# Performance work log

Measured on AMD Instinct MI355X. Metric: run time of the kernel, lower is better.

## Reference

```python
import jax, jax.numpy as jnp
import numpy as np

N_NODES = 50000
N_EDGES = 800000
IN_DIM = 128
HIDDEN = 128
N_CLASSES = 10
BN_EPS = 1e-5


def _sage_conv(x, src, dst, n, w_l, b_l, w_r):
    # PyG SAGEConv (mean aggr): out = lin_l(mean_{j->i} x_j) + lin_r(x_i)
    msg = x[src]  # [E, d] gather
    s = jax.ops.segment_sum(msg, dst, num_segments=n)
    cnt = jax.ops.segment_sum(jnp.ones((src.shape[0], 1), x.dtype), dst, num_segments=n)
    mean = s / jnp.maximum(cnt, 1.0)
    return mean @ w_l.T + b_l + x @ w_r.T


def _bn_eval(x, gamma, beta, mean, var):
    return (x - mean) * (gamma * jax.lax.rsqrt(var + BN_EPS)) + beta


def setup_inputs() -> dict:
    key = jax.random.key(0)
    ks = jax.random.split(key, 16)
    h2 = HIDDEN // 2

    def lin(k, fan_out, fan_in):
        bound = 1.0 / np.sqrt(fan_in)
        return jax.random.uniform(k, (fan_out, fan_in), jnp.float32, -bound, bound)

    return {
        "x": jax.random.normal(ks[0], (N_NODES, IN_DIM), jnp.float32),
        "edge_index": jax.random.randint(ks[1], (2, N_EDGES), 0, N_NODES, jnp.int64),
        "w1l": lin(ks[2], HIDDEN, IN_DIM),
        "b1l": jnp.zeros((HIDDEN,), jnp.float32),
        "w1r": lin(ks[3], HIDDEN, IN_DIM),
        "bn1_gamma": jax.random.uniform(ks[4], (HIDDEN,), jnp.float32, 0.5, 1.5),
        "bn1_beta": jax.random.normal(ks[5], (HIDDEN,), jnp.float32) * 0.1,
        "bn1_mean": jax.random.normal(ks[6], (HIDDEN,), jnp.float32) * 0.1,
        "bn1_var": jax.random.uniform(ks[7], (HIDDEN,), jnp.float32, 0.5, 1.5),
        "w2l": lin(ks[8], h2, HIDDEN),
        "b2l": jnp.zeros((h2,), jnp.float32),
        "w2r": lin(ks[9], h2, HIDDEN),
        "bn2_gamma": jax.random.uniform(ks[10], (h2,), jnp.float32, 0.5, 1.5),
        "bn2_beta": jax.random.normal(ks[11], (h2,), jnp.float32) * 0.1,
        "bn2_mean": jax.random.normal(ks[12], (h2,), jnp.float32) * 0.1,
        "bn2_var": jax.random.uniform(ks[13], (h2,), jnp.float32, 0.5, 1.5),
        "head_w": lin(ks[14], N_CLASSES, h2),
        "head_b": jnp.zeros((N_CLASSES,), jnp.float32),
    }


def reference(x, edge_index, w1l, b1l, w1r, bn1_gamma, bn1_beta, bn1_mean, bn1_var,
              w2l, b2l, w2r, bn2_gamma, bn2_beta, bn2_mean, bn2_var, head_w, head_b):
    src, dst = edge_index[0], edge_index[1]
    n = x.shape[0]
    h = _sage_conv(x, src, dst, n, w1l, b1l, w1r)
    h = jax.nn.relu(_bn_eval(h, bn1_gamma, bn1_beta, bn1_mean, bn1_var))
    # dropout p=0.1 is identity in eval mode
    h = _sage_conv(h, src, dst, n, w2l, b2l, w2r)
    h = jax.nn.relu(_bn_eval(h, bn2_gamma, bn2_beta, bn2_mean, bn2_var))
    return h @ head_w.T + head_b
```

## Files before the change

### kernel.cpp

```cpp
#include <hip/hip_runtime.h>

typedef _Float16 f16;
typedef _Float16 f16x2 __attribute__((ext_vector_type(2)));
typedef _Float16 f16x8 __attribute__((ext_vector_type(8)));
typedef float f32x4 __attribute__((ext_vector_type(4)));

#define N_NODES 50000
#define N_EDGES 800000
#define N_CLASSES 10
#define CAP 64
#define EDGE_BLOCKS ((N_EDGES + 255) / 256)
#define XCVT_BLOCKS (N_NODES * 128 / 8 / 256)

__global__ void zero_cnt_kernel(int* __restrict__ cnt) {
    int i = blockIdx.x * 256 + threadIdx.x;
    if (i < N_NODES / 4) ((int4*)cnt)[i] = make_int4(0, 0, 0, 0);
}

__global__ void build_fused_kernel(const int* __restrict__ src, const int* __restrict__ dst,
                                   int* __restrict__ cnt, unsigned short* __restrict__ bucket,
                                   const float* __restrict__ x,
                                   const float* __restrict__ w1l, const float* __restrict__ w1r,
                                   const float* __restrict__ w2l, const float* __restrict__ w2r,
                                   f16* __restrict__ xh, f16* __restrict__ W1, f16* __restrict__ W2cat) {
    int bid = blockIdx.x;
    if (bid < 2 * EDGE_BLOCKS) {
        int half = bid >> 1;
        if ((bid & 1) == 0) {
            int e = half * 256 + threadIdx.x;
            if (e < N_EDGES) {
                int d = dst[e];
                int s = atomicAdd(&cnt[d], 1);
                if (s < CAP) bucket[(long long)d * CAP + s] = (unsigned short)src[e];
            }
        } else {
            long long base = ((long long)half * 256 + threadIdx.x) * 8;
            float4 a = *(const float4*)(x + base);
            float4 b = *(const float4*)(x + base + 4);
            f16x8 o;
            o[0] = (f16)a.x; o[1] = (f16)a.y; o[2] = (f16)a.z; o[3] = (f16)a.w;
            o[4] = (f16)b.x; o[5] = (f16)b.y; o[6] = (f16)b.z; o[7] = (f16)b.w;
            *(f16x8*)(xh + base) = o;
        }
    } else {
        int wt = (bid - 2 * EDGE_BLOCKS) * 256 + threadIdx.x;
        for (int idx = wt; idx < 128 * 256; idx += 1024) {
            int n = idx >> 8, k = idx & 255;
            W1[idx] = (f16)(k < 128 ? w1l[n * 128 + k] : w1r[n * 128 + k - 128]);
        }
        for (int idx = wt; idx < 128 * 128; idx += 1024) {
            int n = idx >> 7, k = idx & 127;
            W2cat[idx] = (f16)(n < 64 ? w2l[n * 128 + k] : w2r[(n - 64) * 128 + k]);
        }
    }
}

__global__ void agg_mean_f16_kernel(const f16* __restrict__ feat,
                                    const int* __restrict__ cnt,
                                    const unsigned short* __restrict__ bucket,
                                    f16* __restrict__ outb) {
    int node = blockIdx.x * 4 + (threadIdx.x >> 6);
    int lane = threadIdx.x & 63;
    if (node >= N_NODES) return;
    int deg = cnt[node];
    int n_it = deg < CAP ? deg : CAP;
    const unsigned short* b = bucket + (long long)node * CAP;
    int myidx = (lane < n_it) ? (int)b[lane] : 0;
    const f16x2* f2 = (const f16x2*)feat;
    float ax = 0.f, ay = 0.f;
    int j = 0;
    for (; j + 8 <= n_it; j += 8) {
        f16x2 v0 = f2[(long long)__shfl(myidx, j + 0) * 64 + lane];
        f16x2 v1 = f2[(long long)__shfl(myidx, j + 1) * 64 + lane];
        f16x2 v2 = f2[(long long)__shfl(myidx, j + 2) * 64 + lane];
        f16x2 v3 = f2[(long long)__shfl(myidx, j + 3) * 64 + lane];
        f16x2 v4 = f2[(long long)__shfl(myidx, j + 4) * 64 + lane];
        f16x2 v5 = f2[(long long)__shfl(myidx, j + 5) * 64 + lane];
        f16x2 v6 = f2[(long long)__shfl(myidx, j + 6) * 64 + lane];
        f16x2 v7 = f2[(long long)__shfl(myidx, j + 7) * 64 + lane];
        ax += (((float)v0[0] + (float)v1[0]) + ((float)v2[0] + (float)v3[0]))
            + (((float)v4[0] + (float)v5[0]) + ((float)v6[0] + (float)v7[0]));
        ay += (((float)v0[1] + (float)v1[1]) + ((float)v2[1] + (float)v3[1]))
            + (((float)v4[1] + (float)v5[1]) + ((float)v6[1] + (float)v7[1]));
    }
    for (; j + 4 <= n_it; j += 4) {
        f16x2 v0 = f2[(long long)__shfl(myidx, j + 0) * 64 + lane];
        f16x2 v1 = f2[(long long)__shfl(myidx, j + 1) * 64 + lane];
        f16x2 v2 = f2[(long long)__shfl(myidx, j + 2) * 64 + lane];
        f16x2 v3 = f2[(long long)__shfl(myidx, j + 3) * 64 + lane];
        ax += ((float)v0[0] + (float)v1[0]) + ((float)v2[0] + (float)v3[0]);
        ay += ((float)v0[1] + (float)v1[1]) + ((float)v2[1] + (float)v3[1]);
    }
    for (; j < n_it; j++) {
        f16x2 v = f2[(long long)__shfl(myidx, j) * 64 + lane];
        ax += (float)v[0];
        ay += (float)v[1];
    }
    float inv = 1.f / fmaxf((float)deg, 1.f);
    f16x2 r;
    r[0] = (f16)(ax * inv);
    r[1] = (f16)(ay * inv);
    ((f16x2*)outb)[(long long)node * 64 + lane] = r;
}

__global__ __launch_bounds__(256) void sage1_y2_kernel(
    const f16* __restrict__ Am,
    const f16* __restrict__ Ax,
    const f16* __restrict__ W1,
    const float* __restrict__ bias,
    const float* __restrict__ gamma,
    const float* __restrict__ beta,
    const float* __restrict__ bmean,
    const float* __restrict__ bvar,
    const f16* __restrict__ W2cat,
    f16* __restrict__ y2)
{
    __shared__ f16 ldsA[4][32][136];

    int tid  = threadIdx.x;
    int wave = tid >> 6;
    int lane = tid & 63;
    int m_base = blockIdx.x * 128 + wave * 32;
    int lrow = lane & 15;
    int lchunk = lane >> 4;

    f32x4 acc[2][8] = {};

#pragma unroll
    for (int phase = 0; phase < 2; phase++) {
        const f16* A = phase ? Ax : Am;
        const f16* Wp = W1 + phase * 128;

        f16x8 afrag[4][2];
#pragma unroll
        for (int kc = 0; kc < 4; kc++)
#pragma unroll
            for (int mf = 0; mf < 2; mf++) {
                int row = m_base + mf * 16 + lrow;
                row = row < N_NODES ? row : N_NODES - 1;
                afrag[kc][mf] = *(const f16x8*)(A + (long long)row * 128 + kc * 32 + lchunk * 8);
            }

#pragma unroll
        for (int nf = 0; nf < 8; nf++) {
#pragma unroll
            for (int kc = 0; kc < 4; kc++) {
                f16x8 b = *(const f16x8*)(Wp + (long long)(nf * 16 + lrow) * 256
                                          + kc * 32 + lchunk * 8);
                acc[0][nf] = __builtin_amdgcn_mfma_f32_16x16x32_f16(afrag[kc][0], b, acc[0][nf], 0, 0, 0);
                acc[1][nf] = __builtin_amdgcn_mfma_f32_16x16x32_f16(afrag[kc][1], b, acc[1][nf], 0, 0, 0);
            }
        }
    }

#pragma unroll
    for (int nf = 0; nf < 8; nf++) {
        int n = nf * 16 + lrow;
        float mul = gamma[n] * rsqrtf(bvar[n] + 1e-5f);
        float add = (bias[n] - bmean[n]) * mul + beta[n];
#pragma unroll
        for (int mf = 0; mf < 2; mf++) {
#pragma unroll
            for (int r = 0; r < 4; r++) {
                int rloc = mf * 16 + lchunk * 4 + r;
                ldsA[wave][rloc][n] = (f16)fmaxf(fmaf(acc[mf][nf][r], mul, add), 0.f);
            }
        }
    }

#pragma unroll
    for (int nf2 = 0; nf2 < 8; nf2++) {
        f32x4 acc2[2] = {};
#pragma unroll
        for (int kc = 0; kc < 4; kc++) {
            f16x8 b2 = *(const f16x8*)(W2cat + (long long)(nf2 * 16 + lrow) * 128
                                       + kc * 32 + lchunk * 8);
            f16x8 a0 = *(const f16x8*)&ldsA[wave][lrow][kc * 32 + lchunk * 8];
            f16x8 a1 = *(const f16x8*)&ldsA[wave][16 + lrow][kc * 32 + lchunk * 8];
            acc2[0] = __builtin_amdgcn_mfma_f32_16x16x32_f16(a0, b2, acc2[0], 0, 0, 0);
            acc2[1] = __builtin_amdgcn_mfma_f32_16x16x32_f16(a1, b2, acc2[1], 0, 0, 0);
        }
        int n = nf2 * 16 + lrow;
#pragma unroll
        for (int mf = 0; mf < 2; mf++) {
#pragma unroll
            for (int r = 0; r < 4; r++) {
                int m = m_base + mf * 16 + lchunk * 4 + r;
                if (m < N_NODES) y2[(long long)m * 128 + n] = (f16)acc2[mf][r];
            }
        }
    }
}

__global__ void agg_half_kernel(const f16* __restrict__ y2,
                                const int* __restrict__ cnt,
                                const unsigned short* __restrict__ bucket,
                                f16* __restrict__ mean2) {
    int node = blockIdx.x * 4 + (threadIdx.x >> 6);
    int lane = threadIdx.x & 63;
    if (node >= N_NODES) return;
    int deg = cnt[node];
    int n_it = deg < CAP ? deg : CAP;
    const unsigned short* b = bucket + (long long)node * CAP;
    int myidx = (lane < n_it) ? (int)b[lane] : 0;
    float a = 0.f;
    int j = 0;
    for (; j + 8 <= n_it; j += 8) {
        float t0 = (float)y2[(long long)__shfl(myidx, j + 0) * 128 + lane];
        float t1 = (float)y2[(long long)__shfl(myidx, j + 1) * 128 + lane];
        float t2 = (float)y2[(long long)__shfl(myidx, j + 2) * 128 + lane];
        float t3 = (float)y2[(long long)__shfl(myidx, j + 3) * 128 + lane];
        float t4 = (float)y2[(long long)__shfl(myidx, j + 4) * 128 + lane];
        float t5 = (float)y2[(long long)__shfl(myidx, j + 5) * 128 + lane];
        float t6 = (float)y2[(long long)__shfl(myidx, j + 6) * 128 + lane];
        float t7 = (float)y2[(long long)__shfl(myidx, j + 7) * 128 + lane];
        a += ((t0 + t1) + (t2 + t3)) + ((t4 + t5) + (t6 + t7));
    }
    for (; j < n_it; j++)
        a += (float)y2[(long long)__shfl(myidx, j) * 128 + lane];
    mean2[(long long)node * 64 + lane] = (f16)(a / fmaxf((float)deg, 1.f));
}

__global__ void final_head_kernel(const f16* __restrict__ mean2,
                                  const f16* __restrict__ y2,
                                  const float* __restrict__ b2,
                                  const float* __restrict__ gamma,
                                  const float* __restrict__ beta,
                                  const float* __restrict__ bmean,
                                  const float* __restrict__ bvar,
                                  const float* __restrict__ hw,
                                  const float* __restrict__ hb,
                                  float* __restrict__ outp) {
    __shared__ f16 sm[128][68];
    int t = threadIdx.x;
    int rl = t >> 1, hh = t & 1;
    int m = blockIdx.x * 128 + rl;
    if (m < N_NODES) {
        int ch0 = hh * 32;
#pragma unroll
        for (int c = 0; c < 32; c += 8) {
            int ch = ch0 + c;
            f16x8 mv = *(const f16x8*)(mean2 + (long long)m * 64 + ch);
            f16x8 yv = *(const f16x8*)(y2 + (long long)m * 128 + 64 + ch);
#pragma unroll
            for (int i = 0; i < 8; i++) {
                int n = ch + i;
                float mul = gamma[n] * rsqrtf(bvar[n] + 1e-5f);
                float add = (b2[n] - bmean[n]) * mul + beta[n];
                float v = fmaf((float)mv[i] + (float)yv[i], mul, add);
                sm[rl][n] = (f16)fmaxf(v, 0.f);
            }
        }
    }
    __syncthreads();
    if (m < N_NODES) {
        int cb = hh * 5;
        float a0 = hb[cb + 0], a1 = hb[cb + 1], a2 = hb[cb + 2];
        float a3 = hb[cb + 3], a4 = hb[cb + 4];
#pragma unroll 8
        for (int k = 0; k < 64; k++) {
            float hv = (float)sm[rl][k];
            a0 = fmaf(hv, hw[(cb + 0) * 64 + k], a0);
            a1 = fmaf(hv, hw[(cb + 1) * 64 + k], a1);
            a2 = fmaf(hv, hw[(cb + 2) * 64 + k], a2);
            a3 = fmaf(hv, hw[(cb + 3) * 64 + k], a3);
            a4 = fmaf(hv, hw[(cb + 4) * 64 + k], a4);
        }
        float* op = outp + (long long)m * N_CLASSES + cb;
        op[0] = a0; op[1] = a1; op[2] = a2; op[3] = a3; op[4] = a4;
    }
}

extern "C" void kernel_launch(void* const* d_in, const int* in_sizes, int n_in,
                              void* d_out, int out_size, void* d_ws, size_t ws_size,
                              hipStream_t stream) {
    const float* x      = (const float*)d_in[0];
    const int*   ei     = (const int*)d_in[1];
    const float* w1l    = (const float*)d_in[2];
    const float* b1l    = (const float*)d_in[3];
    const float* w1r    = (const float*)d_in[4];
    const float* bn1_g  = (const float*)d_in[5];
    const float* bn1_b  = (const float*)d_in[6];
    const float* bn1_m  = (const float*)d_in[7];
    const float* bn1_v  = (const float*)d_in[8];
    const float* w2l    = (const float*)d_in[9];
    const float* b2l    = (const float*)d_in[10];
    const float* w2r    = (const float*)d_in[11];
    const float* bn2_g  = (const float*)d_in[12];
    const float* bn2_b  = (const float*)d_in[13];
    const float* bn2_m  = (const float*)d_in[14];
    const float* bn2_v  = (const float*)d_in[15];
    const float* head_w = (const float*)d_in[16];
    const float* head_b = (const float*)d_in[17];
    float* out = (float*)d_out;

    const int* src  = ei;
    const int* dstv = ei + N_EDGES;

    char* ws = (char*)d_ws;
    size_t off = 0;
    int* cnt               = (int*)(ws + off); off += ((size_t)N_NODES * 4 + 511) & ~511ull;
    unsigned short* bucket = (unsigned short*)(ws + off); off += (size_t)N_NODES * CAP * 2;
    f16* xh     = (f16*)(ws + off); off += (size_t)N_NODES * 128 * 2;
    f16* meanb  = (f16*)(ws + off); off += (size_t)N_NODES * 128 * 2;
    f16* y2     = (f16*)(ws + off); off += (size_t)N_NODES * 128 * 2;
    f16* mean2  = (f16*)(ws + off); off += (size_t)N_NODES * 64 * 2;
    f16* W1     = (f16*)(ws + off); off += (size_t)128 * 256 * 2;
    f16* W2cat  = (f16*)(ws + off); off += (size_t)128 * 128 * 2;

    zero_cnt_kernel<<<(N_NODES / 4 + 255) / 256, 256, 0, stream>>>(cnt);
    build_fused_kernel<<<2 * EDGE_BLOCKS + 4, 256, 0, stream>>>(
        src, dstv, cnt, bucket, x, w1l, w1r, w2l, w2r, xh, W1, W2cat);

    agg_mean_f16_kernel<<<(N_NODES + 3) / 4, 256, 0, stream>>>(xh, cnt, bucket, meanb);
    sage1_y2_kernel<<<(N_NODES + 127) / 128, 256, 0, stream>>>(
        meanb, xh, W1, b1l, bn1_g, bn1_b, bn1_m, bn1_v, W2cat, y2);

    agg_half_kernel<<<(N_NODES + 3) / 4, 256, 0, stream>>>(y2, cnt, bucket, mean2);
    final_head_kernel<<<(N_NODES + 127) / 128, 256, 0, stream>>>(
        mean2, y2, b2l, bn2_g, bn2_b, bn2_m, bn2_v, head_w, head_b, out);
}
```

Measured before the change: 158.7 us.

## Widen gather loads in aggregation kernels and split sage1 from y2 GEMM

Aggregation kernels now assign 32 or 16 lanes per node with 8-byte f16x4 loads instead of 64 lanes with 2- or 4-byte loads. This packs more nodes per wave and issues fewer, wider gather requests. The fused sage1+y2 kernel is split into two kernels, with the intermediate h1 written to global memory. The split removes LDS staging but adds an extra launch and a full read/write of h1.

Measured after the change: 155.2 us. 2.2% less time.

```diff
diff --git a/kernel.cpp b/kernel.cpp
--- a/kernel.cpp
+++ b/kernel.cpp
@@ -2,6 +2,7 @@
 
 typedef _Float16 f16;
 typedef _Float16 f16x2 __attribute__((ext_vector_type(2)));
+typedef _Float16 f16x4 __attribute__((ext_vector_type(4)));
 typedef _Float16 f16x8 __attribute__((ext_vector_type(8)));
 typedef float f32x4 __attribute__((ext_vector_type(4)));
 
@@ -10,7 +11,6 @@
 #define N_CLASSES 10
 #define CAP 64
 #define EDGE_BLOCKS ((N_EDGES + 255) / 256)
-#define XCVT_BLOCKS (N_NODES * 128 / 8 / 256)
 
 __global__ void zero_cnt_kernel(int* __restrict__ cnt) {
     int i = blockIdx.x * 256 + threadIdx.x;
@@ -59,64 +59,75 @@
                                     const int* __restrict__ cnt,
                                     const unsigned short* __restrict__ bucket,
                                     f16* __restrict__ outb) {
-    int node = blockIdx.x * 4 + (threadIdx.x >> 6);
-    int lane = threadIdx.x & 63;
-    if (node >= N_NODES) return;
+    int node = blockIdx.x * 8 + (threadIdx.x >> 5);
+    int l  = threadIdx.x & 31;
+    int bl = threadIdx.x & 32;
     int deg = cnt[node];
     int n_it = deg < CAP ? deg : CAP;
     const unsigned short* b = bucket + (long long)node * CAP;
-    int myidx = (lane < n_it) ? (int)b[lane] : 0;
-    const f16x2* f2 = (const f16x2*)feat;
-    float ax = 0.f, ay = 0.f;
+    int my0 = (l < n_it)      ? (int)b[l]      : 0;
+    int my1 = (32 + l < n_it) ? (int)b[32 + l] : 0;
+    const f16x4* f4 = (const f16x4*)feat;
+    float a0 = 0.f, a1 = 0.f, a2 = 0.f, a3 = 0.f;
     int j = 0;
+    int lim0 = n_it < 32 ? n_it : 32;
+    for (; j + 8 <= lim0; j += 8) {
+        f16x4 v0 = f4[(long long)__shfl(my0, bl + j + 0) * 32 + l];
+        f16x4 v1 = f4[(long long)__shfl(my0, bl + j + 1) * 32 + l];
+        f16x4 v2 = f4[(long long)__shfl(my0, bl + j + 2) * 32 + l];
+        f16x4 v3 = f4[(long long)__shfl(my0, bl + j + 3) * 32 + l];
+        f16x4 v4 = f4[(long long)__shfl(my0, bl + j + 4) * 32 + l];
+        f16x4 v5 = f4[(long long)__shfl(my0, bl + j + 5) * 32 + l];
+        f16x4 v6 = f4[(long long)__shfl(my0, bl + j + 6) * 32 + l];
+        f16x4 v7 = f4[(long long)__shfl(my0, bl + j + 7) * 32 + l];
+        a0 += (((float)v0[0] + (float)v1[0]) + ((float)v2[0] + (float)v3[0]))
+            + (((float)v4[0] + (float)v5[0]) + ((float)v6[0] + (float)v7[0]));
+        a1 += (((float)v0[1] + (float)v1[1]) + ((float)v2[1] + (float)v3[1]))
+            + (((float)v4[1] + (float)v5[1]) + ((float)v6[1] + (float)v7[1]));
+        a2 += (((float)v0[2] + (float)v1[2]) + ((float)v2[2] + (float)v3[2]))
+            + (((float)v4[2] + (float)v5[2]) + ((float)v6[2] + (float)v7[2]));
+        a3 += (((float)v0[3] + (float)v1[3]) + ((float)v2[3] + (float)v3[3]))
+            + (((float)v4[3] + (float)v5[3]) + ((float)v6[3] + (float)v7[3]));
+    }
+    for (; j < lim0; j++) {
+        f16x4 v = f4[(long long)__shfl(my0, bl + j) * 32 + l];
+        a0 += (float)v[0]; a1 += (float)v[1]; a2 += (float)v[2]; a3 += (float)v[3];
+    }
     for (; j + 8 <= n_it; j += 8) {
-        f16x2 v0 = f2[(long long)__shfl(myidx, j + 0) * 64 + lane];
-        f16x2 v1 = f2[(long long)__shfl(myidx, j + 1) * 64 + lane];
-        f16x2 v2 = f2[(long long)__shfl(myidx, j + 2) * 64 + lane];
-        f16x2 v3 = f2[(long long)__shfl(myidx, j + 3) * 64 + lane];
-        f16x2 v4 = f2[(long long)__shfl(myidx, j + 4) * 64 + lane];
-        f16x2 v5 = f2[(long long)__shfl(myidx, j + 5) * 64 + lane];
-        f16x2 v6 = f2[(long long)__shfl(myidx, j + 6) * 64 + lane];
-        f16x2 v7 = f2[(long long)__shfl(myidx, j + 7) * 64 + lane];
-        ax += (((float)v0[0] + (float)v1[0]) + ((float)v2[0] + (float)v3[0]))
+        f16x4 v0 = f4[(long long)__shfl(my1, bl + j - 32 + 0) * 32 + l];
+        f16x4 v1 = f4[(long long)__shfl(my1, bl + j - 32 + 1) * 32 + l];
+        f16x4 v2 = f4[(long long)__shfl(my1, bl + j - 32 + 2) * 32 + l];
+        f16x4 v3 = f4[(long long)__shfl(my1, bl + j - 32 + 3) * 32 + l];
+        f16x4 v4 = f4[(long long)__shfl(my1, bl + j - 32 + 4) * 32 + l];
+        f16x4 v5 = f4[(long long)__shfl(my1, bl + j - 32 + 5) * 32 + l];
+        f16x4 v6 = f4[(long long)__shfl(my1, bl + j - 32 + 6) * 32 + l];
+        f16x4 v7 = f4[(long long)__shfl(my1, bl + j - 32 + 7) * 32 + l];
+        a0 += (((float)v0[0] + (float)v1[0]) + ((float)v2[0] + (float)v3[0]))
             + (((float)v4[0] + (float)v5[0]) + ((float)v6[0] + (float)v7[0]));
-        ay += (((float)v0[1] + (float)v1[1]) + ((float)v2[1] + (float)v3[1]))
+        a1 += (((float)v0[1] + (float)v1[1]) + ((float)v2[1] + (float)v3[1]))
             + (((float)v4[1] + (float)v5[1]) + ((float)v6[1] + (float)v7[1]));
-    }
-    for (; j + 4 <= n_it; j += 4) {
-        f16x2 v0 = f2[(long long)__shfl(myidx, j + 0) * 64 + lane];
-        f16x2 v1 = f2[(long long)__shfl(myidx, j + 1) * 64 + lane];
-        f16x2 v2 = f2[(long long)__shfl(myidx, j + 2) * 64 + lane];
-        f16x2 v3 = f2[(long long)__shfl(myidx, j + 3) * 64 + lane];
-        ax += ((float)v0[0] + (float)v1[0]) + ((float)v2[0] + (float)v3[0]);
-        ay += ((float)v0[1] + (float)v1[1]) + ((float)v2[1] + (float)v3[1]);
+        a2 += (((float)v0[2] + (float)v1[2]) + ((float)v2[2] + (float)v3[2]))
+            + (((float)v4[2] + (float)v5[2]) + ((float)v6[2] + (float)v7[2]));
+        a3 += (((float)v0[3] + (float)v1[3]) + ((float)v2[3] + (float)v3[3]))
+            + (((float)v4[3] + (float)v5[3]) + ((float)v6[3] + (float)v7[3]));
     }
     for (; j < n_it; j++) {
-        f16x2 v = f2[(long long)__shfl(myidx, j) * 64 + lane];
-        ax += (float)v[0];
-        ay += (float)v[1];
+        f16x4 v = f4[(long long)__shfl(my1, bl + j - 32) * 32 + l];
+        a0 += (float)v[0]; a1 += (float)v[1]; a2 += (float)v[2]; a3 += (float)v[3];
     }
     float inv = 1.f / fmaxf((float)deg, 1.f);
-    f16x2 r;
-    r[0] = (f16)(ax * inv);
-    r[1] = (f16)(ay * inv);
-    ((f16x2*)outb)[(long long)node * 64 + lane] = r;
-}
-
-__global__ __launch_bounds__(256) void sage1_y2_kernel(
-    const f16* __restrict__ Am,
-    const f16* __restrict__ Ax,
+    f16x4 r;
+    r[0] = (f16)(a0 * inv); r[1] = (f16)(a1 * inv);
+    r[2] = (f16)(a2 * inv); r[3] = (f16)(a3 * inv);
+    ((f16x4*)outb)[(long long)node * 32 + l] = r;
+}
+
+__global__ __launch_bounds__(256) void sage1_kernel(
+    const f16* __restrict__ Am, const f16* __restrict__ Ax,
     const f16* __restrict__ W1,
-    const float* __restrict__ bias,
-    const float* __restrict__ gamma,
-    const float* __restrict__ beta,
-    const float* __restrict__ bmean,
-    const float* __restrict__ bvar,
-    const f16* __restrict__ W2cat,
-    f16* __restrict__ y2)
-{
-    __shared__ f16 ldsA[4][32][136];
-
+    const float* __restrict__ bias, const float* __restrict__ gamma,
+    const float* __restrict__ beta, const float* __restrict__ bmean,
+    const float* __restrict__ bvar, f16* __restrict__ C) {
     int tid  = threadIdx.x;
     int wave = tid >> 6;
     int lane = tid & 63;
@@ -130,7 +141,6 @@
     for (int phase = 0; phase < 2; phase++) {
         const f16* A = phase ? Ax : Am;
         const f16* Wp = W1 + phase * 128;
-
         f16x8 afrag[4][2];
 #pragma unroll
         for (int kc = 0; kc < 4; kc++)
@@ -140,9 +150,8 @@
                 row = row < N_NODES ? row : N_NODES - 1;
                 afrag[kc][mf] = *(const f16x8*)(A + (long long)row * 128 + kc * 32 + lchunk * 8);
             }
-
-#pragma unroll
-        for (int nf = 0; nf < 8; nf++) {
+#pragma unroll
+        for (int nf = 0; nf < 8; nf++)
 #pragma unroll
             for (int kc = 0; kc < 4; kc++) {
                 f16x8 b = *(const f16x8*)(Wp + (long long)(nf * 16 + lrow) * 256
@@ -150,7 +159,6 @@
                 acc[0][nf] = __builtin_amdgcn_mfma_f32_16x16x32_f16(afrag[kc][0], b, acc[0][nf], 0, 0, 0);
                 acc[1][nf] = __builtin_amdgcn_mfma_f32_16x16x32_f16(afrag[kc][1], b, acc[1][nf], 0, 0, 0);
             }
-        }
     }
 
 #pragma unroll
@@ -159,36 +167,56 @@
         float mul = gamma[n] * rsqrtf(bvar[n] + 1e-5f);
         float add = (bias[n] - bmean[n]) * mul + beta[n];
 #pragma unroll
-        for (int mf = 0; mf < 2; mf++) {
-#pragma unroll
-            for (int r = 0; r < 4; r++) {
-                int rloc = mf * 16 + lchunk * 4 + r;
-                ldsA[wave][rloc][n] = (f16)fmaxf(fmaf(acc[mf][nf][r], mul, add), 0.f);
-            }
-        }
-    }
-
-#pragma unroll
-    for (int nf2 = 0; nf2 < 8; nf2++) {
-        f32x4 acc2[2] = {};
-#pragma unroll
-        for (int kc = 0; kc < 4; kc++) {
-            f16x8 b2 = *(const f16x8*)(W2cat + (long long)(nf2 * 16 + lrow) * 128
-                                       + kc * 32 + lchunk * 8);
-            f16x8 a0 = *(const f16x8*)&ldsA[wave][lrow][kc * 32 + lchunk * 8];
-            f16x8 a1 = *(const f16x8*)&ldsA[wave][16 + lrow][kc * 32 + lchunk * 8];
-            acc2[0] = __builtin_amdgcn_mfma_f32_16x16x32_f16(a0, b2, acc2[0], 0, 0, 0);
-            acc2[1] = __builtin_amdgcn_mfma_f32_16x16x32_f16(a1, b2, acc2[1], 0, 0, 0);
-        }
-        int n = nf2 * 16 + lrow;
-#pragma unroll
-        for (int mf = 0; mf < 2; mf++) {
+        for (int mf = 0; mf < 2; mf++)
 #pragma unroll
             for (int r = 0; r < 4; r++) {
                 int m = m_base + mf * 16 + lchunk * 4 + r;
-                if (m < N_NODES) y2[(long long)m * 128 + n] = (f16)acc2[mf][r];
-            }
-        }
+                if (m < N_NODES) {
+                    float v = fmaxf(fmaf(acc[mf][nf][r], mul, add), 0.f);
+                    C[(long long)m * 128 + n] = (f16)v;
+                }
+            }
+    }
+}
+
+__global__ __launch_bounds__(256) void y2_kernel(const f16* __restrict__ h1,
+                                                 const f16* __restrict__ W2cat,
+                                                 f16* __restrict__ y2) {
+    int tid  = threadIdx.x;
+    int wave = tid >> 6;
+    int lane = tid & 63;
+    int m_base = blockIdx.x * 128 + wave * 32;
+    int lrow = lane & 15;
+    int lchunk = lane >> 4;
+
+    f16x8 afrag[4][2];
+#pragma unroll
+    for (int kc = 0; kc < 4; kc++)
+#pragma unroll
+        for (int mf = 0; mf < 2; mf++) {
+            int row = m_base + mf * 16 + lrow;
+            row = row < N_NODES ? row : N_NODES - 1;
+            afrag[kc][mf] = *(const f16x8*)(h1 + (long long)row * 128 + kc * 32 + lchunk * 8);
+        }
+
+#pragma unroll
+    for (int nf = 0; nf < 8; nf++) {
+        f32x4 acc[2] = {};
+#pragma unroll
+        for (int kc = 0; kc < 4; kc++) {
+            f16x8 b = *(const f16x8*)(W2cat + (long long)(nf * 16 + lrow) * 128
+                                      + kc * 32 + lchunk * 8);
+            acc[0] = __builtin_amdgcn_mfma_f32_16x16x32_f16(afrag[kc][0], b, acc[0], 0, 0, 0);
+            acc[1] = __builtin_amdgcn_mfma_f32_16x16x32_f16(afrag[kc][1], b, acc[1], 0, 0, 0);
+        }
+        int n = nf * 16 + lrow;
+#pragma unroll
+        for (int mf = 0; mf < 2; mf++)
+#pragma unroll
+            for (int r = 0; r < 4; r++) {
+                int m = m_base + mf * 16 + lchunk * 4 + r;
+                if (m < N_NODES) y2[(long long)m * 128 + n] = (f16)acc[mf][r];
+            }
     }
 }
 
@@ -196,29 +224,59 @@
                                 const int* __restrict__ cnt,
                                 const unsigned short* __restrict__ bucket,
                                 f16* __restrict__ mean2) {
-    int node = blockIdx.x * 4 + (threadIdx.x >> 6);
-    int lane = threadIdx.x & 63;
-    if (node >= N_NODES) return;
+    int node = blockIdx.x * 16 + (threadIdx.x >> 4);
+    int l  = threadIdx.x & 15;
+    int bl = threadIdx.x & 48;
     int deg = cnt[node];
     int n_it = deg < CAP ? deg : CAP;
     const unsigned short* b = bucket + (long long)node * CAP;
-    int myidx = (lane < n_it) ? (int)b[lane] : 0;
-    float a = 0.f;
+    int my0 = (l < n_it)      ? (int)b[l]      : 0;
+    int my1 = (16 + l < n_it) ? (int)b[16 + l] : 0;
+    int my2 = (32 + l < n_it) ? (int)b[32 + l] : 0;
+    int my3 = (48 + l < n_it) ? (int)b[48 + l] : 0;
+    const f16x4* f4 = (const f16x4*)y2;
+    float a0 = 0.f, a1 = 0.f, a2 = 0.f, a3 = 0.f;
     int j = 0;
-    for (; j + 8 <= n_it; j += 8) {
-        float t0 = (float)y2[(long long)__shfl(myidx, j + 0) * 128 + lane];
-        float t1 = (float)y2[(long long)__shfl(myidx, j + 1) * 128 + lane];
-        float t2 = (float)y2[(long long)__shfl(myidx, j + 2) * 128 + lane];
-        float t3 = (float)y2[(long long)__shfl(myidx, j + 3) * 128 + lane];
-        float t4 = (float)y2[(long long)__shfl(myidx, j + 4) * 128 + lane];
-        float t5 = (float)y2[(long long)__shfl(myidx, j + 5) * 128 + lane];
-        float t6 = (float)y2[(long long)__shfl(myidx, j + 6) * 128 + lane];
-        float t7 = (float)y2[(long long)__shfl(myidx, j + 7) * 128 + lane];
-        a += ((t0 + t1) + (t2 + t3)) + ((t4 + t5) + (t6 + t7));
-    }
-    for (; j < n_it; j++)
-        a += (float)y2[(long long)__shfl(myidx, j) * 128 + lane];
-    mean2[(long long)node * 64 + lane] = (f16)(a / fmaxf((float)deg, 1.f));
+
+#define AGG_SEC(MYREG, BASE)                                                     \
+    {                                                                            \
+        int lim = n_it < (BASE + 16) ? n_it : (BASE + 16);                       \
+        for (; j + 8 <= lim; j += 8) {                                           \
+            f16x4 v0 = f4[(long long)__shfl(MYREG, bl + j - BASE + 0) * 32 + l]; \
+            f16x4 v1 = f4[(long long)__shfl(MYREG, bl + j - BASE + 1) * 32 + l]; \
+            f16x4 v2 = f4[(long long)__shfl(MYREG, bl + j - BASE + 2) * 32 + l]; \
+            f16x4 v3 = f4[(long long)__shfl(MYREG, bl + j - BASE + 3) * 32 + l]; \
+            f16x4 v4 = f4[(long long)__shfl(MYREG, bl + j - BASE + 4) * 32 + l]; \
+            f16x4 v5 = f4[(long long)__shfl(MYREG, bl + j - BASE + 5) * 32 + l]; \
+            f16x4 v6 = f4[(long long)__shfl(MYREG, bl + j - BASE + 6) * 32 + l]; \
+            f16x4 v7 = f4[(long long)__shfl(MYREG, bl + j - BASE + 7) * 32 + l]; \
+            a0 += (((float)v0[0] + (float)v1[0]) + ((float)v2[0] + (float)v3[0]))\
+                + (((float)v4[0] + (float)v5[0]) + ((float)v6[0] + (float)v7[0]));\
+            a1 += (((float)v0[1] + (float)v1[1]) + ((float)v2[1] + (float)v3[1]))\
+                + (((float)v4[1] + (float)v5[1]) + ((float)v6[1] + (float)v7[1]));\
+            a2 += (((float)v0[2] + (float)v1[2]) + ((float)v2[2] + (float)v3[2]))\
+                + (((float)v4[2] + (float)v5[2]) + ((float)v6[2] + (float)v7[2]));\
+            a3 += (((float)v0[3] + (float)v1[3]) + ((float)v2[3] + (float)v3[3]))\
+                + (((float)v4[3] + (float)v5[3]) + ((float)v6[3] + (float)v7[3]));\
+        }                                                                        \
+        for (; j < lim; j++) {                                                   \
+            f16x4 v = f4[(long long)__shfl(MYREG, bl + j - BASE) * 32 + l];      \
+            a0 += (float)v[0]; a1 += (float)v[1];                                \
+            a2 += (float)v[2]; a3 += (float)v[3];                                \
+        }                                                                        \
+    }
+
+    AGG_SEC(my0, 0)
+    AGG_SEC(my1, 16)
+    AGG_SEC(my2, 32)
+    AGG_SEC(my3, 48)
+#undef AGG_SEC
+
+    float inv = 1.f / fmaxf((float)deg, 1.f);
+    f16x4 r;
+    r[0] = (f16)(a0 * inv); r[1] = (f16)(a1 * inv);
+    r[2] = (f16)(a2 * inv); r[3] = (f16)(a3 * inv);
+    ((f16x4*)mean2)[(long long)node * 16 + l] = r;
 }
 
 __global__ void final_head_kernel(const f16* __restrict__ mean2,
@@ -303,6 +361,7 @@
     unsigned short* bucket = (unsigned short*)(ws + off); off += (size_t)N_NODES * CAP * 2;
     f16* xh     = (f16*)(ws + off); off += (size_t)N_NODES * 128 * 2;
     f16* meanb  = (f16*)(ws + off); off += (size_t)N_NODES * 128 * 2;
+    f16* h1     = (f16*)(ws + off); off += (size_t)N_NODES * 128 * 2;
     f16* y2     = (f16*)(ws + off); off += (size_t)N_NODES * 128 * 2;
     f16* mean2  = (f16*)(ws + off); off += (size_t)N_NODES * 64 * 2;
     f16* W1     = (f16*)(ws + off); off += (size_t)128 * 256 * 2;
@@ -312,11 +371,12 @@
     build_fused_kernel<<<2 * EDGE_BLOCKS + 4, 256, 0, stream>>>(
         src, dstv, cnt, bucket, x, w1l, w1r, w2l, w2r, xh, W1, W2cat);
 
-    agg_mean_f16_kernel<<<(N_NODES + 3) / 4, 256, 0, stream>>>(xh, cnt, bucket, meanb);
-    sage1_y2_kernel<<<(N_NODES + 127) / 128, 256, 0, stream>>>(
-        meanb, xh, W1, b1l, bn1_g, bn1_b, bn1_m, bn1_v, W2cat, y2);
-
-    agg_half_kernel<<<(N_NODES + 3) / 4, 256, 0, stream>>>(y2, cnt, bucket, mean2);
+    agg_mean_f16_kernel<<<N_NODES / 8, 256, 0, stream>>>(xh, cnt, bucket, meanb);
+    sage1_kernel<<<(N_NODES + 127) / 128, 256, 0, stream>>>(
+        meanb, xh, W1, b1l, bn1_g, bn1_b, bn1_m, bn1_v, h1);
+
+    y2_kernel<<<(N_NODES + 127) / 128, 256, 0, stream>>>(h1, W2cat, y2);
+    agg_half_kernel<<<N_NODES / 16, 256, 0, stream>>>(y2, cnt, bucket, mean2);
     final_head_kernel<<<(N_NODES + 127) / 128, 256, 0, stream>>>(
         mean2, y2, b2l, bn2_g, bn2_b, bn2_m, bn2_v, head_w, head_b, out);
 }
```
